# Performance work log

Measured on AMD Instinct MI355X. Metric: run time of the kernel, lower is better.

Reference implementation:

```python
import jax, jax.numpy as jnp
import numpy as np

EPS = 1e-12  # F.normalize eps

def _l2norm(x, axis=-1):
    n = jnp.sqrt(jnp.sum(x * x, axis=axis, keepdims=True))
    return x / jnp.maximum(n, EPS)

def setup_inputs() -> dict:
    key = jax.random.key(0)
    k1, k2, k3, k4 = jax.random.split(key, 4)
    B, S, L, E, H = 16, 4096, 512, 1024, 1024
    return {
        'input_data': jax.random.normal(k1, (B, S, H), dtype=jnp.float32),
        'label_repr': jax.random.normal(k2, (B, L, E), dtype=jnp.float32),
        'W_proj': jax.random.normal(k3, (H, E), dtype=jnp.float32) * (1.0 / np.sqrt(E)),
        'padding_mask': jax.random.randint(k4, (B, S), 0, 2, dtype=jnp.int32),
    }

def reference(input_data, label_repr, W_proj, padding_mask):
    # project labels: [B, L, E] @ [E, H] -> [B, L, H]
    lab = jnp.einsum('ble,he->blh', label_repr, W_proj)
    x_n = _l2norm(input_data, axis=-1)        # [B, S, H]
    lab_n = _l2norm(lab, axis=-1)             # [B, L, H] (== normalize dim=1 after transpose)
    G = jnp.einsum('bsh,blh->bsl', x_n, lab_n)  # cosine scores [B, S, L]
    mask = (padding_mask == 0)[:, :, None]    # True where padded
    G = jnp.where(mask, -jnp.inf, G)
    softmax_G = jax.nn.softmax(G, axis=1)     # softmax over sequence axis
    output = jnp.einsum('bsl,bsh->blh', softmax_G, x_n)  # [B, L, H]
    return (output, softmax_G)
```

## Files before the change

### kernel.cpp

```cpp
#include <hip/hip_runtime.h>
#include <hip/hip_bf16.h>
#include <cmath>

#define B_DIM 16
#define S_DIM 4096
#define L_DIM 512
#define E_DIM 1024
#define H_DIM 1024

typedef __bf16 bf16;
typedef __attribute__((ext_vector_type(8))) __bf16 bf16x8;
typedef __attribute__((ext_vector_type(4))) __bf16 bf16x4;
typedef __attribute__((ext_vector_type(4))) float f32x4;
typedef __attribute__((ext_vector_type(8))) unsigned short u16x8;

__device__ __forceinline__ void gload_lds16(const void* g, void* l) {
  __builtin_amdgcn_global_load_lds((const __attribute__((address_space(1))) void*)g,
                                   (__attribute__((address_space(3))) void*)l,
                                   16, 0, 0);
}

#define SWZ(o) ((o) ^ ((((o) >> 9) & 1) << 5))

__global__ void k_cast(const float* __restrict__ in, bf16* __restrict__ out, int n4) {
  int stride = gridDim.x * blockDim.x;
  for (int i = blockIdx.x * blockDim.x + threadIdx.x; i < n4; i += stride) {
    float4 v = reinterpret_cast<const float4*>(in)[i];
    bf16x4 o = { (bf16)v.x, (bf16)v.y, (bf16)v.z, (bf16)v.w };
    reinterpret_cast<bf16x4*>(out)[i] = o;
  }
}

__global__ __launch_bounds__(256) void k_rownorm_f32(const float* __restrict__ in,
                                                     bf16* __restrict__ out) {
  const size_t r = blockIdx.x;
  const int t = threadIdx.x;
  const float4 v = reinterpret_cast<const float4*>(in + r * 1024)[t];
  float ss = v.x * v.x + v.y * v.y + v.z * v.z + v.w * v.w;
#pragma unroll
  for (int off = 32; off; off >>= 1) ss += __shfl_xor(ss, off);
  __shared__ float red[4];
  if ((t & 63) == 0) red[t >> 6] = ss;
  __syncthreads();
  const float tot = red[0] + red[1] + red[2] + red[3];
  const float inv = 1.0f / fmaxf(sqrtf(tot), 1e-12f);
  bf16x4 o = { (bf16)(v.x * inv), (bf16)(v.y * inv), (bf16)(v.z * inv), (bf16)(v.w * inv) };
  reinterpret_cast<bf16x4*>(out + r * 1024)[t] = o;
}

__global__ __launch_bounds__(256) void k_rownorm_add(const float* __restrict__ P,
                                                     bf16* __restrict__ out) {
  const int r = blockIdx.x;
  const int b = r >> 9, l = r & 511;
  const int t = threadIdx.x;
  const float* p0 = P + ((size_t)b * 1024 + l) * 1024;
  const float4 v0 = reinterpret_cast<const float4*>(p0)[t];
  const float4 v1 = reinterpret_cast<const float4*>(p0 + 524288)[t];
  const float4 v = make_float4(v0.x + v1.x, v0.y + v1.y, v0.z + v1.z, v0.w + v1.w);
  float ss = v.x * v.x + v.y * v.y + v.z * v.z + v.w * v.w;
#pragma unroll
  for (int off = 32; off; off >>= 1) ss += __shfl_xor(ss, off);
  __shared__ float red[4];
  if ((t & 63) == 0) red[t >> 6] = ss;
  __syncthreads();
  const float tot = red[0] + red[1] + red[2] + red[3];
  const float inv = 1.0f / fmaxf(sqrtf(tot), 1e-12f);
  bf16x4 o = { (bf16)(v.x * inv), (bf16)(v.y * inv), (bf16)(v.z * inv), (bf16)(v.w * inv) };
  reinterpret_cast<bf16x4*>(out + (size_t)r * 1024)[t] = o;
}

__global__ void k_addout(const float* __restrict__ P, float* __restrict__ out, int total4,
                         int LH4) {
  int stride = gridDim.x * blockDim.x;
  for (int i = blockIdx.x * blockDim.x + threadIdx.x; i < total4; i += stride) {
    int b = i / LH4, rem = i - b * LH4;
    const float4* p0 = reinterpret_cast<const float4*>(P) + (size_t)b * 2 * LH4 + rem;
    float4 a = p0[0], c = p0[LH4];
    reinterpret_cast<float4*>(out)[i] = make_float4(a.x + c.x, a.y + c.y, a.z + c.z, a.w + c.w);
  }
}

__global__ __launch_bounds__(256) void k_transpose(const bf16* __restrict__ in,
                                                   bf16* __restrict__ out, int R, int C) {
  __shared__ unsigned short tile[64][72];
  const int r0 = blockIdx.x * 64, c0 = blockIdx.y * 64;
  const size_t boff = (size_t)blockIdx.z * (size_t)R * C;
  const unsigned short* src = (const unsigned short*)in + boff;
  unsigned short* dst = (unsigned short*)out + boff;
  const int t = threadIdx.x;
#pragma unroll
  for (int p = 0; p < 2; ++p) {
    int r = p * 32 + (t >> 3);
    int c = (t & 7) * 8;
    u16x8 v = *reinterpret_cast<const u16x8*>(src + (size_t)(r0 + r) * C + c0 + c);
#pragma unroll
    for (int j = 0; j < 8; ++j) tile[r][c + j] = v[j];
  }
  __syncthreads();
#pragma unroll
  for (int p = 0; p < 2; ++p) {
    int cc = p * 32 + (t >> 3);
    int rr = (t & 7) * 8;
    u16x8 o;
#pragma unroll
    for (int j = 0; j < 8; ++j) o[j] = tile[rr + j][cc];
    *reinterpret_cast<u16x8*>(dst + (size_t)(c0 + cc) * R + r0 + rr) = o;
  }
}

template <int OUT_BF16, int KSPLIT>
__global__ __launch_bounds__(512, 2) void k_gemm8(const bf16* __restrict__ Aall,
                                                  const bf16* __restrict__ Ball,
                                                  void* __restrict__ Call, const int N,
                                                  const int ldk, const int Klen,
                                                  const size_t sA, const size_t sB,
                                                  const size_t sC) {
  extern __shared__ char lds[];
  const int z = blockIdx.z;
  const int b = z / KSPLIT, ks = z - b * KSPLIT;
  const int koff = ks * Klen;
  const int t = threadIdx.x, wid = t >> 6, lane = t & 63;
  const int wm = wid >> 2, wn = wid & 3;
  const int lane_r = lane & 15;
  const int lane_k = (lane >> 4) * 16;
  const int row0 = blockIdx.y * 256, col0 = blockIdx.x * 256;
  const bf16* srcA = Aall + (size_t)b * sA + (size_t)row0 * ldk + koff;
  const bf16* srcB = Ball + (size_t)b * sB + (size_t)col0 * ldk + koff;
  const int NKT = Klen >> 6;

  int s_r[2], s_ce[2];
#pragma unroll
  for (int li = 0; li < 2; ++li) {
    int o = li * 8192 + t * 16;
    int so = SWZ(o);
    s_r[li] = so >> 7;
    s_ce[li] = (so & 127) >> 1;
  }

  f32x4 acc[8][4];
#pragma unroll
  for (int i = 0; i < 8; ++i)
#pragma unroll
    for (int j = 0; j < 4; ++j) acc[i][j] = (f32x4){0.f, 0.f, 0.f, 0.f};

  bf16x8 aq[4][2], b0[2][2], b1[2][2];

  auto STAGE = [&](int c, int isB, int h, const bf16* src, int kt_idx) {
#pragma unroll
    for (int li = 0; li < 2; ++li) {
      const bf16* g = src + (size_t)(h * 128 + s_r[li]) * ldk + (kt_idx * 64 + s_ce[li]);
      char* d = lds + c * 65536 + isB * 32768 + h * 16384 + li * 8192 + wid * 1024;
      gload_lds16(g, d);
    }
  };
  auto LDA = [&](int c, int mh) {
#pragma unroll
    for (int mi = 0; mi < 4; ++mi)
#pragma unroll
      for (int kk = 0; kk < 2; ++kk) {
        int rl = (mh * 4 + mi) * 16 + lane_r;
        int o = rl * 128 + lane_k + kk * 64;
        aq[mi][kk] =
            *reinterpret_cast<const bf16x8*>(lds + c * 65536 + wm * 16384 + SWZ(o));
      }
  };
  auto LDB = [&](int c, int nh, bf16x8(&bq)[2][2]) {
#pragma unroll
    for (int ni = 0; ni < 2; ++ni)
#pragma unroll
      for (int kk = 0; kk < 2; ++kk) {
        int rl = (wn & 1) * 64 + (nh * 2 + ni) * 16 + lane_r;
        int o = rl * 128 + lane_k + kk * 64;
        bq[ni][kk] = *reinterpret_cast<const bf16x8*>(lds + c * 65536 + 32768 +
                                                      (wn >> 1) * 16384 + SWZ(o));
      }
  };
  auto MMA = [&](int mh, int nh, bf16x8(&bq)[2][2]) {
#pragma unroll
    for (int mi = 0; mi < 4; ++mi)
#pragma unroll
      for (int ni = 0; ni < 2; ++ni)
#pragma unroll
        for (int kk = 0; kk < 2; ++kk)
          acc[mh * 4 + mi][nh * 2 + ni] = __builtin_amdgcn_mfma_f32_16x16x32_bf16(
              aq[mi][kk], bq[ni][kk], acc[mh * 4 + mi][nh * 2 + ni], 0, 0, 0);
  };

#define GS_BEGIN                                        \
  __builtin_amdgcn_s_barrier();                         \
  asm volatile("s_waitcnt lgkmcnt(0)" ::: "memory");    \
  __builtin_amdgcn_sched_barrier(0);                    \
  __builtin_amdgcn_s_setprio(1);
#define GS_END                                          \
  __builtin_amdgcn_s_setprio(0);                        \
  __builtin_amdgcn_s_barrier();

  STAGE(0, 0, 0, srcA, 0);
  STAGE(0, 1, 0, srcB, 0);
  STAGE(0, 0, 1, srcA, 0);
  STAGE(0, 1, 1, srcB, 0);
  STAGE(1, 0, 0, srcA, 1);
  STAGE(1, 1, 0, srcB, 1);
  STAGE(1, 0, 1, srcA, 1);
  asm volatile("s_waitcnt vmcnt(6)" ::: "memory");
  __builtin_amdgcn_s_barrier();

#pragma unroll 1
  for (int kt = 0; kt < NKT; kt += 2) {
    const bool s2 = kt + 2 < NKT, s3 = kt + 3 < NKT;
    LDA(0, 0);
    LDB(0, 0, b0);
    STAGE(1, 1, 1, srcB, kt + 1);
    GS_BEGIN; MMA(0, 0, b0); GS_END;
    LDB(0, 1, b1);
    GS_BEGIN; MMA(0, 1, b1); GS_END;
    LDA(0, 1);
    if (s2) STAGE(0, 1, 0, srcB, kt + 2);
    GS_BEGIN; MMA(1, 1, b1); GS_END;
    if (s2) {
      STAGE(0, 0, 0, srcA, kt + 2);
      asm volatile("s_waitcnt vmcnt(4)" ::: "memory");
    } else {
      asm volatile("s_waitcnt vmcnt(0)" ::: "memory");
    }
    GS_BEGIN; MMA(1, 0, b0); GS_END;
    LDA(1, 0);
    LDB(1, 0, b0);
    if (s2) STAGE(0, 1, 1, srcB, kt + 2);
    GS_BEGIN; MMA(0, 0, b0); GS_END;
    LDB(1, 1, b1);
    if (s2) STAGE(0, 0, 1, srcA, kt + 2);
    GS_BEGIN; MMA(0, 1, b1); GS_END;
    LDA(1, 1);
    if (s3) STAGE(1, 1, 0, srcB, kt + 3);
    GS_BEGIN; MMA(1, 1, b1); GS_END;
    if (s3) {
      STAGE(1, 0, 0, srcA, kt + 3);
      STAGE(1, 0, 1, srcA, kt + 3);
      asm volatile("s_waitcnt vmcnt(6)" ::: "memory");
    } else {
      asm volatile("s_waitcnt vmcnt(0)" ::: "memory");
    }
    GS_BEGIN; MMA(1, 0, b0); GS_END;
  }
#undef GS_BEGIN
#undef GS_END

  const int rb = row0 + wm * 128 + (lane >> 4) * 4;
  const int cb = col0 + wn * 64 + lane_r;
  if (OUT_BF16) {
    bf16* C = (bf16*)Call + (size_t)z * sC;
#pragma unroll
    for (int mf = 0; mf < 8; ++mf)
#pragma unroll
      for (int nf = 0; nf < 4; ++nf)
#pragma unroll
        for (int r = 0; r < 4; ++r)
          C[(size_t)(rb + mf * 16 + r) * N + cb + nf * 16] = (bf16)acc[mf][nf][r];
  } else {
    float* C = (float*)Call + (size_t)z * sC;
#pragma unroll
    for (int mf = 0; mf < 8; ++mf)
#pragma unroll
      for (int nf = 0; nf < 4; ++nf)
#pragma unroll
        for (int r = 0; r < 4; ++r)
          C[(size_t)(rb + mf * 16 + r) * N + cb + nf * 16] = acc[mf][nf][r];
  }
}

__global__ __launch_bounds__(256) void k_sm_part(const bf16* __restrict__ GT,
                                                 const int* __restrict__ mask,
                                                 float2* __restrict__ part) {
  const int b = blockIdx.z, lt = blockIdx.y, sc = blockIdx.x;
  const int t = threadIdx.x, w = t >> 6, lane = t & 63;
  const int s_base = sc * 512;
  bool valid[8];
#pragma unroll
  for (int q = 0; q < 8; ++q)
    valid[q] = (mask[(size_t)b * S_DIM + s_base + q * 64 + lane] != 0);
  for (int i = 0; i < 16; ++i) {
    const int l = lt * 64 + w * 16 + i;
    const bf16* row = GT + ((size_t)b * L_DIM + l) * S_DIM + s_base;
    float m = -INFINITY, z = 0.f;
#pragma unroll
    for (int q = 0; q < 8; ++q) {
      float g = valid[q] ? (float)row[q * 64 + lane] : -INFINITY;
      float mn = fmaxf(m, g);
      if (mn != -INFINITY) {
        z = z * __expf(m - mn) + __expf(g - mn);
        m = mn;
      }
    }
#pragma unroll
    for (int off = 32; off; off >>= 1) {
      float mo = __shfl_xor(m, off);
      float zo = __shfl_xor(z, off);
      float mn = fmaxf(m, mo);
      if (mn != -INFINITY) {
        z = z * __expf(m - mn) + zo * __expf(mo - mn);
      } else {
        z = 0.f;
      }
      m = mn;
    }
    if (lane == 0) part[((size_t)b * L_DIM + l) * 8 + sc] = make_float2(m, z);
  }
}

__global__ void k_sm_comb(const float2* __restrict__ part, float2* __restrict__ mz, int n) {
  int id = blockIdx.x * blockDim.x + threadIdx.x;
  if (id >= n) return;
  float2 p[8];
#pragma unroll
  for (int q = 0; q < 8; ++q) p[q] = part[(size_t)id * 8 + q];
  float M = -INFINITY;
#pragma unroll
  for (int q = 0; q < 8; ++q) M = fmaxf(M, p[q].x);
  float Z = 0.f;
  if (M != -INFINITY) {
#pragma unroll
    for (int q = 0; q < 8; ++q)
      if (p[q].x != -INFINITY) Z += p[q].y * __expf(p[q].x - M);
  }
  float rZ = (Z > 0.f) ? 1.0f / Z : 0.f;
  mz[id] = make_float2(M, rZ);
}

__global__ __launch_bounds__(256) void k_sm_write(bf16* __restrict__ GT,
                                                  const int* __restrict__ mask,
                                                  const float2* __restrict__ mz,
                                                  float* __restrict__ out1) {
  __shared__ float tile[64][65];
  const int b = blockIdx.z, lt = blockIdx.y, sc = blockIdx.x;
  const int t = threadIdx.x, w = t >> 6, lane = t & 63;
  const int s_base = sc * 512;
  for (int st = 0; st < 8; ++st) {
    const int s_tile = s_base + st * 64;
    const bool v = (mask[(size_t)b * S_DIM + s_tile + lane] != 0);
#pragma unroll
    for (int i = 0; i < 16; ++i) {
      const int l = lt * 64 + w * 16 + i;
      const float2 mzv = mz[(size_t)b * L_DIM + l];
      bf16* rp = GT + ((size_t)b * L_DIM + l) * S_DIM + s_tile + lane;
      const float g = (float)*rp;
      const float p = (v && mzv.x != -INFINITY) ? __expf(g - mzv.x) * mzv.y : 0.f;
      *rp = (bf16)p;
      tile[lane][w * 16 + i] = p;
    }
    __syncthreads();
#pragma unroll
    for (int q = 0; q < 16; ++q) {
      const int s_local = q * 4 + w;
      out1[((size_t)b * S_DIM + s_tile + s_local) * L_DIM + lt * 64 + lane] =
          tile[s_local][lane];
    }
    __syncthreads();
  }
}

extern "C" void kernel_launch(void* const* d_in, const int* in_sizes, int n_in, void* d_out,
                              int out_size, void* d_ws, size_t ws_size, hipStream_t stream) {
  const float* input_data = (const float*)d_in[0];
  const float* label_repr = (const float*)d_in[1];
  const float* W_proj = (const float*)d_in[2];
  const int* padding = (const int*)d_in[3];
  float* out0 = (float*)d_out;
  float* out1 = out0 + (size_t)B_DIM * L_DIM * H_DIM;

  char* ws = (char*)d_ws;
  bf16* xn = (bf16*)(ws + 0);
  bf16* xnT = (bf16*)(ws + 134217728);
  bf16* labb = (bf16*)(ws + 268435456);
  bf16* Wb = (bf16*)(ws + 285212672);
  bf16* lab = (bf16*)(ws + 287309824);
  bf16* GT = (bf16*)(ws + 304087040);
  float2* part = (float2*)(ws + 371195904);
  float2* mz = (float2*)(ws + 371720192);
  float* Pk2 = (float*)(ws + 304087040);
  float* Pk5 = (float*)(ws + 0);

  (void)hipFuncSetAttribute((const void*)k_gemm8<0, 2>,
                            hipFuncAttributeMaxDynamicSharedMemorySize, 131072);
  (void)hipFuncSetAttribute((const void*)k_gemm8<1, 1>,
                            hipFuncAttributeMaxDynamicSharedMemorySize, 131072);

  k_cast<<<2048, 256, 0, stream>>>(label_repr, labb, (B_DIM * L_DIM * E_DIM) / 4);
  k_cast<<<512, 256, 0, stream>>>(W_proj, Wb, (H_DIM * E_DIM) / 4);
  k_rownorm_f32<<<B_DIM * S_DIM, 256, 0, stream>>>(input_data, xn);
  k_transpose<<<dim3(S_DIM / 64, H_DIM / 64, B_DIM), 256, 0, stream>>>(xn, xnT, S_DIM, H_DIM);
  k_gemm8<0, 2><<<dim3(H_DIM / 256, L_DIM / 256, B_DIM * 2), 512, 131072, stream>>>(
      labb, Wb, Pk2, H_DIM, E_DIM, 512, (size_t)L_DIM * E_DIM, 0, (size_t)L_DIM * H_DIM);
  k_rownorm_add<<<B_DIM * L_DIM, 256, 0, stream>>>(Pk2, lab);
  k_gemm8<1, 1><<<dim3(S_DIM / 256, L_DIM / 256, B_DIM), 512, 131072, stream>>>(
      lab, xn, GT, S_DIM, H_DIM, H_DIM, (size_t)L_DIM * H_DIM, (size_t)S_DIM * H_DIM,
      (size_t)L_DIM * S_DIM);
  k_sm_part<<<dim3(8, 8, B_DIM), 256, 0, stream>>>(GT, padding, part);
  k_sm_comb<<<(B_DIM * L_DIM + 255) / 256, 256, 0, stream>>>(part, mz, B_DIM * L_DIM);
  k_sm_write<<<dim3(8, 8, B_DIM), 256, 0, stream>>>(GT, padding, mz, out1);
  k_gemm8<0, 2><<<dim3(H_DIM / 256, L_DIM / 256, B_DIM * 2), 512, 131072, stream>>>(
      GT, xnT, Pk5, H_DIM, S_DIM, 2048, (size_t)L_DIM * S_DIM, (size_t)H_DIM * S_DIM,
      (size_t)L_DIM * H_DIM);
  k_addout<<<2048, 256, 0, stream>>>(Pk5, out0, (B_DIM * L_DIM * H_DIM) / 4,
                                     (L_DIM * H_DIM) / 4);
}
```

Before: 482.8 us.

## Fuse softmax partial stats into score GEMM, remap grid, wave-per-row norms

The score GEMM epilogue now computes per-row max and sum-exp over its 256-column tile, using fp32 accumulators and the padding mask. It writes 16 partials per row, which removes the separate k_sm_part pass that re-read the bf16 score matrix. All GEMM launches switch to a 1D grid with an XCD-aware block remapping (bid&7 striding), intended to improve L2 locality on MI355X. The row-norm kernels become grid-stride, one wave per row with no shared-memory reduction. Partials now come from fp32 values instead of the rounded bf16 scores, so they differ slightly from what is written, and the epilogue gains extra shuffles and a barrier.

```diff
diff --git a/kernel.cpp b/kernel.cpp
--- a/kernel.cpp
+++ b/kernel.cpp
@@ -32,41 +32,61 @@
 }
 
 __global__ __launch_bounds__(256) void k_rownorm_f32(const float* __restrict__ in,
-                                                     bf16* __restrict__ out) {
-  const size_t r = blockIdx.x;
-  const int t = threadIdx.x;
-  const float4 v = reinterpret_cast<const float4*>(in + r * 1024)[t];
-  float ss = v.x * v.x + v.y * v.y + v.z * v.z + v.w * v.w;
-#pragma unroll
-  for (int off = 32; off; off >>= 1) ss += __shfl_xor(ss, off);
-  __shared__ float red[4];
-  if ((t & 63) == 0) red[t >> 6] = ss;
-  __syncthreads();
-  const float tot = red[0] + red[1] + red[2] + red[3];
-  const float inv = 1.0f / fmaxf(sqrtf(tot), 1e-12f);
-  bf16x4 o = { (bf16)(v.x * inv), (bf16)(v.y * inv), (bf16)(v.z * inv), (bf16)(v.w * inv) };
-  reinterpret_cast<bf16x4*>(out + r * 1024)[t] = o;
+                                                     bf16* __restrict__ out, int nrows) {
+  const int wave = (blockIdx.x * 256 + threadIdx.x) >> 6;
+  const int lane = threadIdx.x & 63;
+  const int nw = (gridDim.x * 256) >> 6;
+  for (int r = wave; r < nrows; r += nw) {
+    const float4* src = reinterpret_cast<const float4*>(in + (size_t)r * 1024);
+    float4 v[4];
+    float ss = 0.f;
+#pragma unroll
+    for (int j = 0; j < 4; ++j) {
+      v[j] = src[lane + j * 64];
+      ss += v[j].x * v[j].x + v[j].y * v[j].y + v[j].z * v[j].z + v[j].w * v[j].w;
+    }
+#pragma unroll
+    for (int off = 32; off; off >>= 1) ss += __shfl_xor(ss, off);
+    const float inv = 1.0f / fmaxf(sqrtf(ss), 1e-12f);
+    bf16x4* dst = reinterpret_cast<bf16x4*>(out + (size_t)r * 1024);
+#pragma unroll
+    for (int j = 0; j < 4; ++j) {
+      bf16x4 o = { (bf16)(v[j].x * inv), (bf16)(v[j].y * inv), (bf16)(v[j].z * inv),
+                   (bf16)(v[j].w * inv) };
+      dst[lane + j * 64] = o;
+    }
+  }
 }
 
 __global__ __launch_bounds__(256) void k_rownorm_add(const float* __restrict__ P,
-                                                     bf16* __restrict__ out) {
-  const int r = blockIdx.x;
-  const int b = r >> 9, l = r & 511;
-  const int t = threadIdx.x;
-  const float* p0 = P + ((size_t)b * 1024 + l) * 1024;
-  const float4 v0 = reinterpret_cast<const float4*>(p0)[t];
-  const float4 v1 = reinterpret_cast<const float4*>(p0 + 524288)[t];
-  const float4 v = make_float4(v0.x + v1.x, v0.y + v1.y, v0.z + v1.z, v0.w + v1.w);
-  float ss = v.x * v.x + v.y * v.y + v.z * v.z + v.w * v.w;
-#pragma unroll
-  for (int off = 32; off; off >>= 1) ss += __shfl_xor(ss, off);
-  __shared__ float red[4];
-  if ((t & 63) == 0) red[t >> 6] = ss;
-  __syncthreads();
-  const float tot = red[0] + red[1] + red[2] + red[3];
-  const float inv = 1.0f / fmaxf(sqrtf(tot), 1e-12f);
-  bf16x4 o = { (bf16)(v.x * inv), (bf16)(v.y * inv), (bf16)(v.z * inv), (bf16)(v.w * inv) };
-  reinterpret_cast<bf16x4*>(out + (size_t)r * 1024)[t] = o;
+                                                     bf16* __restrict__ out, int nrows) {
+  const int wave = (blockIdx.x * 256 + threadIdx.x) >> 6;
+  const int lane = threadIdx.x & 63;
+  const int nw = (gridDim.x * 256) >> 6;
+  for (int r = wave; r < nrows; r += nw) {
+    const int b = r >> 9, l = r & 511;
+    const float* p0 = P + ((size_t)b * 1024 + l) * 1024;
+    const float4* s0 = reinterpret_cast<const float4*>(p0);
+    const float4* s1 = reinterpret_cast<const float4*>(p0 + 524288);
+    float4 v[4];
+    float ss = 0.f;
+#pragma unroll
+    for (int j = 0; j < 4; ++j) {
+      float4 a = s0[lane + j * 64], c = s1[lane + j * 64];
+      v[j] = make_float4(a.x + c.x, a.y + c.y, a.z + c.z, a.w + c.w);
+      ss += v[j].x * v[j].x + v[j].y * v[j].y + v[j].z * v[j].z + v[j].w * v[j].w;
+    }
+#pragma unroll
+    for (int off = 32; off; off >>= 1) ss += __shfl_xor(ss, off);
+    const float inv = 1.0f / fmaxf(sqrtf(ss), 1e-12f);
+    bf16x4* dst = reinterpret_cast<bf16x4*>(out + (size_t)r * 1024);
+#pragma unroll
+    for (int j = 0; j < 4; ++j) {
+      bf16x4 o = { (bf16)(v[j].x * inv), (bf16)(v[j].y * inv), (bf16)(v[j].z * inv),
+                   (bf16)(v[j].w * inv) };
+      dst[lane + j * 64] = o;
+    }
+  }
 }
 
 __global__ void k_addout(const float* __restrict__ P, float* __restrict__ out, int total4,
@@ -108,22 +128,26 @@
   }
 }
 
-template <int OUT_BF16, int KSPLIT>
-__global__ __launch_bounds__(512, 2) void k_gemm8(const bf16* __restrict__ Aall,
-                                                  const bf16* __restrict__ Ball,
-                                                  void* __restrict__ Call, const int N,
-                                                  const int ldk, const int Klen,
-                                                  const size_t sA, const size_t sB,
-                                                  const size_t sC) {
+template <int MODE, int KSPLIT>
+__global__ __launch_bounds__(512, 2) void k_gemm8(
+    const bf16* __restrict__ Aall, const bf16* __restrict__ Ball, void* __restrict__ Call,
+    const int N, const int ldk, const int Klen, const size_t sA, const size_t sB,
+    const size_t sC, const int lg_nbx, const int* __restrict__ mask,
+    float2* __restrict__ part) {
   extern __shared__ char lds[];
-  const int z = blockIdx.z;
+  const int bid = blockIdx.x, ntot = gridDim.x;
+  const int wg = (bid & 7) * (ntot >> 3) + (bid >> 3);
+  const int by = wg & 1;
+  const int tmp2 = wg >> 1;
+  const int bx = tmp2 & ((1 << lg_nbx) - 1);
+  const int z = tmp2 >> lg_nbx;
   const int b = z / KSPLIT, ks = z - b * KSPLIT;
   const int koff = ks * Klen;
   const int t = threadIdx.x, wid = t >> 6, lane = t & 63;
   const int wm = wid >> 2, wn = wid & 3;
   const int lane_r = lane & 15;
   const int lane_k = (lane >> 4) * 16;
-  const int row0 = blockIdx.y * 256, col0 = blockIdx.x * 256;
+  const int row0 = by * 256, col0 = bx * 256;
   const bf16* srcA = Aall + (size_t)b * sA + (size_t)row0 * ldk + koff;
   const bf16* srcB = Ball + (size_t)b * sB + (size_t)col0 * ldk + koff;
   const int NKT = Klen >> 6;
@@ -248,7 +272,7 @@
 
   const int rb = row0 + wm * 128 + (lane >> 4) * 4;
   const int cb = col0 + wn * 64 + lane_r;
-  if (OUT_BF16) {
+  if (MODE == 2) {
     bf16* C = (bf16*)Call + (size_t)z * sC;
 #pragma unroll
     for (int mf = 0; mf < 8; ++mf)
@@ -257,6 +281,41 @@
 #pragma unroll
         for (int r = 0; r < 4; ++r)
           C[(size_t)(rb + mf * 16 + r) * N + cb + nf * 16] = (bf16)acc[mf][nf][r];
+    bool vld[4];
+#pragma unroll
+    for (int nf = 0; nf < 4; ++nf)
+      vld[nf] = mask[(size_t)b * N + col0 + wn * 64 + nf * 16 + lane_r] != 0;
+    float2* smb = reinterpret_cast<float2*>(lds);
+#pragma unroll
+    for (int mf = 0; mf < 8; ++mf)
+#pragma unroll
+      for (int r = 0; r < 4; ++r) {
+        float m = -INFINITY;
+#pragma unroll
+        for (int nf = 0; nf < 4; ++nf)
+          if (vld[nf]) m = fmaxf(m, acc[mf][nf][r]);
+#pragma unroll
+        for (int off = 1; off < 16; off <<= 1) m = fmaxf(m, __shfl_xor(m, off));
+        float zz = 0.f;
+#pragma unroll
+        for (int nf = 0; nf < 4; ++nf)
+          if (vld[nf]) zz += __expf(acc[mf][nf][r] - m);
+#pragma unroll
+        for (int off = 1; off < 16; off <<= 1) zz += __shfl_xor(zz, off);
+        if (lane_r == 0)
+          smb[(wm * 128 + mf * 16 + (lane >> 4) * 4 + r) * 4 + wn] = make_float2(m, zz);
+      }
+    __syncthreads();
+    if (t < 256) {
+      float2 p0 = smb[t * 4 + 0], p1 = smb[t * 4 + 1], p2 = smb[t * 4 + 2],
+             p3 = smb[t * 4 + 3];
+      float M = fmaxf(fmaxf(p0.x, p1.x), fmaxf(p2.x, p3.x));
+      float Z = 0.f;
+      if (M != -INFINITY)
+        Z = p0.y * __expf(p0.x - M) + p1.y * __expf(p1.x - M) + p2.y * __expf(p2.x - M) +
+            p3.y * __expf(p3.x - M);
+      part[((size_t)b * L_DIM + row0 + t) * 16 + bx] = make_float2(M, Z);
+    }
   } else {
     float* C = (float*)Call + (size_t)z * sC;
 #pragma unroll
@@ -266,61 +325,23 @@
 #pragma unroll
         for (int r = 0; r < 4; ++r)
           C[(size_t)(rb + mf * 16 + r) * N + cb + nf * 16] = acc[mf][nf][r];
-  }
-}
-
-__global__ __launch_bounds__(256) void k_sm_part(const bf16* __restrict__ GT,
-                                                 const int* __restrict__ mask,
-                                                 float2* __restrict__ part) {
-  const int b = blockIdx.z, lt = blockIdx.y, sc = blockIdx.x;
-  const int t = threadIdx.x, w = t >> 6, lane = t & 63;
-  const int s_base = sc * 512;
-  bool valid[8];
-#pragma unroll
-  for (int q = 0; q < 8; ++q)
-    valid[q] = (mask[(size_t)b * S_DIM + s_base + q * 64 + lane] != 0);
-  for (int i = 0; i < 16; ++i) {
-    const int l = lt * 64 + w * 16 + i;
-    const bf16* row = GT + ((size_t)b * L_DIM + l) * S_DIM + s_base;
-    float m = -INFINITY, z = 0.f;
-#pragma unroll
-    for (int q = 0; q < 8; ++q) {
-      float g = valid[q] ? (float)row[q * 64 + lane] : -INFINITY;
-      float mn = fmaxf(m, g);
-      if (mn != -INFINITY) {
-        z = z * __expf(m - mn) + __expf(g - mn);
-        m = mn;
-      }
-    }
-#pragma unroll
-    for (int off = 32; off; off >>= 1) {
-      float mo = __shfl_xor(m, off);
-      float zo = __shfl_xor(z, off);
-      float mn = fmaxf(m, mo);
-      if (mn != -INFINITY) {
-        z = z * __expf(m - mn) + zo * __expf(mo - mn);
-      } else {
-        z = 0.f;
-      }
-      m = mn;
-    }
-    if (lane == 0) part[((size_t)b * L_DIM + l) * 8 + sc] = make_float2(m, z);
   }
 }
 
 __global__ void k_sm_comb(const float2* __restrict__ part, float2* __restrict__ mz, int n) {
   int id = blockIdx.x * blockDim.x + threadIdx.x;
   if (id >= n) return;
-  float2 p[8];
-#pragma unroll
-  for (int q = 0; q < 8; ++q) p[q] = part[(size_t)id * 8 + q];
+  float2 p[16];
   float M = -INFINITY;
 #pragma unroll
-  for (int q = 0; q < 8; ++q) M = fmaxf(M, p[q].x);
+  for (int q = 0; q < 16; ++q) {
+    p[q] = part[(size_t)id * 16 + q];
+    M = fmaxf(M, p[q].x);
+  }
   float Z = 0.f;
   if (M != -INFINITY) {
 #pragma unroll
-    for (int q = 0; q < 8; ++q)
+    for (int q = 0; q < 16; ++q)
       if (p[q].x != -INFINITY) Z += p[q].y * __expf(p[q].x - M);
   }
   float rZ = (Z > 0.f) ? 1.0f / Z : 0.f;
@@ -376,31 +397,31 @@
   bf16* lab = (bf16*)(ws + 287309824);
   bf16* GT = (bf16*)(ws + 304087040);
   float2* part = (float2*)(ws + 371195904);
-  float2* mz = (float2*)(ws + 371720192);
+  float2* mz = (float2*)(ws + 372244480);
   float* Pk2 = (float*)(ws + 304087040);
   float* Pk5 = (float*)(ws + 0);
 
   (void)hipFuncSetAttribute((const void*)k_gemm8<0, 2>,
                             hipFuncAttributeMaxDynamicSharedMemorySize, 131072);
-  (void)hipFuncSetAttribute((const void*)k_gemm8<1, 1>,
+  (void)hipFuncSetAttribute((const void*)k_gemm8<2, 1>,
                             hipFuncAttributeMaxDynamicSharedMemorySize, 131072);
 
   k_cast<<<2048, 256, 0, stream>>>(label_repr, labb, (B_DIM * L_DIM * E_DIM) / 4);
   k_cast<<<512, 256, 0, stream>>>(W_proj, Wb, (H_DIM * E_DIM) / 4);
-  k_rownorm_f32<<<B_DIM * S_DIM, 256, 0, stream>>>(input_data, xn);
+  k_rownorm_f32<<<2048, 256, 0, stream>>>(input_data, xn, B_DIM * S_DIM);
   k_transpose<<<dim3(S_DIM / 64, H_DIM / 64, B_DIM), 256, 0, stream>>>(xn, xnT, S_DIM, H_DIM);
-  k_gemm8<0, 2><<<dim3(H_DIM / 256, L_DIM / 256, B_DIM * 2), 512, 131072, stream>>>(
-      labb, Wb, Pk2, H_DIM, E_DIM, 512, (size_t)L_DIM * E_DIM, 0, (size_t)L_DIM * H_DIM);
-  k_rownorm_add<<<B_DIM * L_DIM, 256, 0, stream>>>(Pk2, lab);
-  k_gemm8<1, 1><<<dim3(S_DIM / 256, L_DIM / 256, B_DIM), 512, 131072, stream>>>(
-      lab, xn, GT, S_DIM, H_DIM, H_DIM, (size_t)L_DIM * H_DIM, (size_t)S_DIM * H_DIM,
-      (size_t)L_DIM * S_DIM);
-  k_sm_part<<<dim3(8, 8, B_DIM), 256, 0, stream>>>(GT, padding, part);
+  k_gemm8<0, 2><<<256, 512, 131072, stream>>>(labb, Wb, Pk2, H_DIM, E_DIM, 512,
+                                              (size_t)L_DIM * E_DIM, 0,
+                                              (size_t)L_DIM * H_DIM, 2, nullptr, nullptr);
+  k_rownorm_add<<<512, 256, 0, stream>>>(Pk2, lab, B_DIM * L_DIM);
+  k_gemm8<2, 1><<<512, 512, 131072, stream>>>(lab, xn, GT, S_DIM, H_DIM, H_DIM,
+                                              (size_t)L_DIM * H_DIM, (size_t)S_DIM * H_DIM,
+                                              (size_t)L_DIM * S_DIM, 4, padding, part);
   k_sm_comb<<<(B_DIM * L_DIM + 255) / 256, 256, 0, stream>>>(part, mz, B_DIM * L_DIM);
   k_sm_write<<<dim3(8, 8, B_DIM), 256, 0, stream>>>(GT, padding, mz, out1);
-  k_gemm8<0, 2><<<dim3(H_DIM / 256, L_DIM / 256, B_DIM * 2), 512, 131072, stream>>>(
-      GT, xnT, Pk5, H_DIM, S_DIM, 2048, (size_t)L_DIM * S_DIM, (size_t)H_DIM * S_DIM,
-      (size_t)L_DIM * H_DIM);
+  k_gemm8<0, 2><<<256, 512, 131072, stream>>>(GT, xnT, Pk5, H_DIM, S_DIM, 2048,
+                                              (size_t)L_DIM * S_DIM, (size_t)H_DIM * S_DIM,
+                                              (size_t)L_DIM * H_DIM, 2, nullptr, nullptr);
   k_addout<<<2048, 256, 0, stream>>>(Pk5, out0, (B_DIM * L_DIM * H_DIM) / 4,
                                      (L_DIM * H_DIM) / 4);
 }
```

After: 460.6 us. 1.05x faster.
